# Kernel optimization log

Measured on AMD Instinct MI355X. Metric: run time of the kernel, lower is better.

The kernel has to match this reference:

```python
import jax, jax.numpy as jnp
import numpy as np

N = 100000
E = 1600000
F_IN, F_HID, F_OUT = 512, 512, 256
NEG_SLOPE = 0.01  # nn.LeakyReLU default


def setup_inputs() -> dict:
    key = jax.random.key(0)
    ks = jax.random.split(key, 16)
    def lin(k, fi, fo):
        s = 1.0 / np.sqrt(fi)
        return jax.random.uniform(k, (fi, fo), jnp.float32, -s, s)
    inp = {
        'x': jax.random.normal(ks[0], (N, F_IN), jnp.float32),
        'edge_index': jax.random.randint(ks[1], (2, E), 0, N, jnp.int64),
        'W1': lin(ks[2], F_IN, F_HID), 'b1': jnp.zeros((F_HID,), jnp.float32),
        'W2': lin(ks[3], F_HID, F_HID), 'b2': jnp.zeros((F_HID,), jnp.float32),
        'W3': lin(ks[4], F_HID, F_HID), 'b3': jnp.zeros((F_HID,), jnp.float32),
        'W4': lin(ks[5], F_HID, F_OUT), 'b4': jnp.zeros((F_OUT,), jnp.float32),
        'fcW1': lin(ks[6], F_OUT, 64), 'fcb1': jnp.zeros((64,), jnp.float32),
        'fcW2': lin(ks[7], 64, 1), 'fcb2': jnp.zeros((1,), jnp.float32),
    }
    return inp


def _gcn_norm(edge_index):
    # PyG gcn_norm with add_self_loops=True: deg counts incoming edges + 1 self loop
    src, dst = edge_index[0], edge_index[1]
    deg = jax.ops.segment_sum(jnp.ones((E,), jnp.float32), dst, num_segments=N) + 1.0
    dis = jax.lax.rsqrt(deg)  # deg >= 1 always (self loops)
    edge_norm = dis[src] * dis[dst]  # [E]
    self_norm = dis * dis            # [N], norm for the added self loop
    return src, dst, edge_norm, self_norm


def _gcn_layer(x, src, dst, edge_norm, self_norm, W, b):
    xw = x @ W  # transform-then-propagate (in < out not an issue here)
    agg = jax.ops.segment_sum(xw[src] * edge_norm[:, None], dst, num_segments=N)
    return agg + self_norm[:, None] * xw + b


def leaky(x):
    return jnp.where(x >= 0, x, NEG_SLOPE * x)


def reference(x, edge_index, W1, b1, W2, b2, W3, b3, W4, b4, fcW1, fcb1, fcW2, fcb2):
    src, dst, en, sn = _gcn_norm(edge_index)
    h = leaky(_gcn_layer(x, src, dst, en, sn, W1, b1))
    h = leaky(_gcn_layer(h, src, dst, en, sn, W2, b2))
    h = leaky(_gcn_layer(h, src, dst, en, sn, W3, b3))
    h = leaky(_gcn_layer(h, src, dst, en, sn, W4, b4))
    g = jnp.mean(h, axis=0, keepdims=True)  # global_mean_pool, batch=None -> [1, F_OUT]
    g = leaky(g @ fcW1 + fcb1)
    # dropout is identity in eval mode
    g = g @ fcW2 + fcb2
    return jax.nn.sigmoid(g)  # [1, 1]
```

## Files before the change

kernel.cpp:

```cpp
#include <hip/hip_runtime.h>
#include <hip/hip_bf16.h>
#include <cstdint>
#include <cstddef>


typedef unsigned short u16;
typedef unsigned char u8;
typedef unsigned int u32;
typedef u16 u16x4 __attribute__((ext_vector_type(4)));
typedef u16 u16x8 __attribute__((ext_vector_type(8)));
typedef u32 u32x2 __attribute__((ext_vector_type(2)));
typedef float f32x2 __attribute__((ext_vector_type(2)));
typedef float f32x4 __attribute__((ext_vector_type(4)));

__device__ __forceinline__ u16 f2bf(float f) {
  u32 u = __builtin_bit_cast(u32, f);
  u += 0x7fffu + ((u >> 16) & 1u);
  return (u16)(u >> 16);
}
__device__ __forceinline__ float bf2f(u16 h) {
  return __builtin_bit_cast(float, (u32)h << 16);
}
__device__ __forceinline__ void g2lds16(const void* g, void* l) {
  __builtin_amdgcn_global_load_lds((__attribute__((address_space(1))) void*)g,
                                   (__attribute__((address_space(3))) void*)l, 16, 0, 0);
}

__global__ __launch_bounds__(256) void init_kernel(int* __restrict__ deg,
                                                   int* __restrict__ cursor,
                                                   float* __restrict__ pool, int N) {
  int i = blockIdx.x * 256 + threadIdx.x;
  if (i < N) { deg[i] = 0; cursor[i] = 0; }
  if (i < 256) pool[i] = 0.f;
}

__global__ void detect_kernel(const int* __restrict__ ei, int* __restrict__ flag) {
  __shared__ int nz;
  if (threadIdx.x == 0) nz = 0;
  __syncthreads();
  if (ei[2 * threadIdx.x + 1] != 0) atomicAdd(&nz, 1);
  __syncthreads();
  if (threadIdx.x == 0) *flag = (nz == 0) ? 1 : 0;
}

__device__ __forceinline__ int ld_src(const int* ei, int E, int e, int f64) {
  return f64 ? (int)((const long long*)ei)[e] : ei[e];
}
__device__ __forceinline__ int ld_dst(const int* ei, int E, int e, int f64) {
  return f64 ? (int)((const long long*)ei)[(long long)E + e] : ei[E + e];
}

__global__ __launch_bounds__(256) void degree_kernel(const int* __restrict__ ei,
                                                     const int* __restrict__ flag,
                                                     int* __restrict__ deg, int E) {
  int e = blockIdx.x * 256 + threadIdx.x;
  if (e >= E) return;
  int f = *flag;
  atomicAdd(&deg[ld_dst(ei, E, e, f)], 1);
}

__global__ __launch_bounds__(256) void dis_kernel(const int* __restrict__ deg,
                                                  float* __restrict__ dis, int N) {
  int i = blockIdx.x * 256 + threadIdx.x;
  if (i < N) dis[i] = rsqrtf((float)deg[i] + 1.0f);
}

__global__ __launch_bounds__(1024) void scan1_kernel(const int* __restrict__ deg,
                                                     int* __restrict__ rs,
                                                     int* __restrict__ bsum, int N) {
  __shared__ int s[1024];
  int tid = threadIdx.x;
  int i = blockIdx.x * 1024 + tid;
  int v = (i < N) ? deg[i] : 0;
  s[tid] = v;
  __syncthreads();
  for (int off = 1; off < 1024; off <<= 1) {
    int t = (tid >= off) ? s[tid - off] : 0;
    __syncthreads();
    s[tid] += t;
    __syncthreads();
  }
  if (i < N) rs[i] = s[tid] - v;
  if (tid == 1023) bsum[blockIdx.x] = s[1023];
}

__global__ __launch_bounds__(1024) void scan2_kernel(const int* __restrict__ bsum,
                                                     int* __restrict__ boff, int nb) {
  __shared__ int s[1024];
  int tid = threadIdx.x;
  int v = (tid < nb) ? bsum[tid] : 0;
  s[tid] = v;
  __syncthreads();
  for (int off = 1; off < 1024; off <<= 1) {
    int t = (tid >= off) ? s[tid - off] : 0;
    __syncthreads();
    s[tid] += t;
    __syncthreads();
  }
  if (tid < nb) boff[tid] = s[tid] - v;
}

__global__ __launch_bounds__(256) void scan3_kernel(int* __restrict__ rs,
                                                    const int* __restrict__ boff, int N) {
  int i = blockIdx.x * 256 + threadIdx.x;
  if (i < N) rs[i] += boff[i >> 10];
}

__global__ __launch_bounds__(256) void fill_kernel(const int* __restrict__ ei,
                                                   const int* __restrict__ flag,
                                                   const int* __restrict__ rs,
                                                   int* __restrict__ cursor,
                                                   const float* __restrict__ dis,
                                                   u32x2* __restrict__ ev, int E) {
  int e = blockIdx.x * 256 + threadIdx.x;
  if (e >= E) return;
  int f = *flag;
  int s = ld_src(ei, E, e, f);
  int d = ld_dst(ei, E, e, f);
  int p = atomicAdd(&cursor[d], 1);
  float w = dis[s] * dis[d];
  u32x2 t;
  t.x = (u32)s;
  t.y = __builtin_bit_cast(u32, w);
  ev[rs[d] + p] = t;
}

__global__ __launch_bounds__(256) void convx_kernel(const float* __restrict__ x,
                                                    u8* __restrict__ x8, size_t n) {
  size_t i = ((size_t)blockIdx.x * 256 + threadIdx.x) * 4;
  if (i >= n) return;
  float4 v = *reinterpret_cast<const float4*>(x + i);
  int lo = __builtin_amdgcn_cvt_pk_fp8_f32(v.x, v.y, 0, false);
  int r = __builtin_amdgcn_cvt_pk_fp8_f32(v.z, v.w, lo, true);
  size_t row = i >> 9;
  int col = (int)(i & 511);
  int sw = ((int)(row & 7)) << 3;
  *reinterpret_cast<u32*>(x8 + row * 512 + (col ^ sw)) = (u32)r;
}

__global__ __launch_bounds__(256) void convw_kernel(const float* __restrict__ W,
                                                    u8* __restrict__ Wt, int Nout) {
  int id = blockIdx.x * 256 + threadIdx.x;
  if (id >= 512 * Nout) return;
  int k = id / Nout, nn = id - k * Nout;
  float v = W[id];
  int e = __builtin_amdgcn_cvt_pk_fp8_f32(v, v, 0, false);
  Wt[nn * 512 + (k ^ ((nn & 7) << 3))] = (u8)e;
}

__global__ __launch_bounds__(256, 4)
void gemm8_kernel(const u8* __restrict__ A, const u8* __restrict__ Bt,
                  u8* __restrict__ Cout, int M, int Nout, int gm, int lgy) {
  const int id = blockIdx.x;
  const int xcd = id & 7, q = id >> 3;
  const int by = q & ((1 << lgy) - 1);
  const int bx = ((q >> lgy) << 3) + xcd;
  if (bx >= gm) return;

  __shared__ u8 sA[128 * 64];
  __shared__ u8 sB[128 * 64];
  const int tid = threadIdx.x;
  const int wave = tid >> 6, lane = tid & 63;
  const int m0 = bx * 128;
  const int n0 = by * 128;
  const int wm = (wave >> 1) * 64, wn = (wave & 1) * 64;
  const int srow = tid >> 2;
  const int soff = (tid & 3) * 16;
  const int fr = lane & 15, fq8 = (lane >> 4) * 8;
  const int xa = (fr & 7) << 3;

  f32x4 acc[4][4];
#pragma unroll
  for (int i = 0; i < 4; ++i)
#pragma unroll
    for (int j = 0; j < 4; ++j) acc[i][j] = (f32x4){0.f, 0.f, 0.f, 0.f};

  int ar0 = m0 + srow;      if (ar0 >= M) ar0 = M - 1;
  int ar1 = m0 + 64 + srow; if (ar1 >= M) ar1 = M - 1;
  const size_t a0 = (size_t)ar0 * 512 + soff;
  const size_t a1 = (size_t)ar1 * 512 + soff;
  const size_t b0 = (size_t)(n0 + srow) * 512 + soff;
  const size_t b1 = (size_t)(n0 + 64 + srow) * 512 + soff;

  for (int k0 = 0; k0 < 512; k0 += 64) {
    g2lds16(A + a0 + k0, &sA[wave * 1024]);
    g2lds16(A + a1 + k0, &sA[4096 + wave * 1024]);
    g2lds16(Bt + b0 + k0, &sB[wave * 1024]);
    g2lds16(Bt + b1 + k0, &sB[4096 + wave * 1024]);
    __builtin_amdgcn_s_waitcnt(0);
    __syncthreads();

#pragma unroll
    for (int s = 0; s < 2; ++s) {
      long long af[4], bf[4];
#pragma unroll
      for (int t = 0; t < 4; ++t) {
        const int ra = (wm + t * 16 + fr) * 64;
        const int rb = (wn + t * 16 + fr) * 64;
        af[t] = *reinterpret_cast<const long long*>(&sA[ra + ((s * 32 + fq8) ^ xa)]);
        bf[t] = *reinterpret_cast<const long long*>(&sB[rb + ((s * 32 + fq8) ^ xa)]);
      }
#pragma unroll
      for (int i = 0; i < 4; ++i)
#pragma unroll
        for (int j = 0; j < 4; ++j)
          acc[i][j] = __builtin_amdgcn_mfma_f32_16x16x32_fp8_fp8(af[i], bf[j], acc[i][j], 0, 0, 0);
    }
    __syncthreads();
  }

  const int crow0 = m0 + wm + ((lane >> 4) << 2);
  const int ccol0 = n0 + wn + (lane & 15);
#pragma unroll
  for (int j = 0; j < 4; ++j) {
    const int col = ccol0 + j * 16;
#pragma unroll
    for (int i = 0; i < 4; ++i)
#pragma unroll
      for (int r = 0; r < 4; ++r) {
        int row = crow0 + i * 16 + r;
        if (row < M) {
          float v = acc[i][j][r];
          int e = __builtin_amdgcn_cvt_pk_fp8_f32(v, v, 0, false);
          Cout[(size_t)row * Nout + col] = (u8)e;
        }
      }
  }
}

__global__ __launch_bounds__(256)
void agg_kernel(const u8* __restrict__ xw, const u32x2* __restrict__ ev,
                const int* __restrict__ rs, const int* __restrict__ deg,
                const float* __restrict__ dis, const float* __restrict__ bias,
                u8* __restrict__ hout, int N) {
  const int wave = threadIdx.x >> 6;
  const int lane = threadIdx.x & 63;
  const int node = blockIdx.x * 4 + wave;
  if (node >= N) return;
  const int start = rs[node];
  const int d = deg[node];
  const float dd = dis[node];
  const int fo = lane * 8;

  f32x2 acc[4];
#pragma unroll
  for (int i = 0; i < 4; ++i) acc[i] = (f32x2){0.f, 0.f};

  const int total = d + 1;
  for (int base = 0; base < total; base += 64) {
    int t = base + lane;
    int s = node;
    float w = 0.f;
    if (t < d)       { u32x2 e = ev[start + t]; s = (int)e.x; w = __builtin_bit_cast(float, e.y); }
    else if (t == d) { w = dd * dd; }
    int cnt = total - base;
    if (cnt > 64) cnt = 64;
    int cnt8 = (cnt + 7) & ~7;
    int wi = __builtin_bit_cast(int, w);
    for (int j = 0; j < cnt8; j += 8) {
      u32x2 v[8];
      float ws[8];
#pragma unroll
      for (int k = 0; k < 8; ++k) {
        int sk = __builtin_amdgcn_readlane(s, j + k);
        ws[k] = __builtin_bit_cast(float, __builtin_amdgcn_readlane(wi, j + k));
        v[k] = *reinterpret_cast<const u32x2*>(xw + (size_t)sk * 512 + fo);
      }
#pragma unroll
      for (int k = 0; k < 8; ++k) {
        f32x2 p0 = __builtin_amdgcn_cvt_pk_f32_fp8((int)v[k].x, false);
        f32x2 p1 = __builtin_amdgcn_cvt_pk_f32_fp8((int)v[k].x, true);
        f32x2 p2 = __builtin_amdgcn_cvt_pk_f32_fp8((int)v[k].y, false);
        f32x2 p3 = __builtin_amdgcn_cvt_pk_f32_fp8((int)v[k].y, true);
        f32x2 wv = (f32x2){ws[k], ws[k]};
        acc[0] += wv * p0;
        acc[1] += wv * p1;
        acc[2] += wv * p2;
        acc[3] += wv * p3;
      }
    }
  }

  float h[8];
#pragma unroll
  for (int i = 0; i < 8; ++i) {
    float v = (i & 1) ? acc[i >> 1].y : acc[i >> 1].x;
    v += bias[fo + i];
    v = v >= 0.f ? v : 0.01f * v;
    h[i] = v;
  }
  int lo = __builtin_amdgcn_cvt_pk_fp8_f32(h[0], h[1], 0, false);
  lo = __builtin_amdgcn_cvt_pk_fp8_f32(h[2], h[3], lo, true);
  int hi = __builtin_amdgcn_cvt_pk_fp8_f32(h[4], h[5], 0, false);
  hi = __builtin_amdgcn_cvt_pk_fp8_f32(h[6], h[7], hi, true);
  u32x2 o; o.x = (u32)lo; o.y = (u32)hi;
  __builtin_nontemporal_store(o, reinterpret_cast<u32x2*>(
      hout + (size_t)node * 512 + (fo ^ ((node & 7) << 3))));
}

__global__ __launch_bounds__(256)
void agg256_kernel(const u8* __restrict__ xw, const u32x2* __restrict__ ev,
                   const int* __restrict__ rs, const int* __restrict__ deg,
                   const float* __restrict__ dis, const float* __restrict__ bias,
                   u16* __restrict__ hout, int N) {
  const int wave = threadIdx.x >> 6;
  const int lane = threadIdx.x & 63;
  const int node = blockIdx.x * 4 + wave;
  if (node >= N) return;
  const int start = rs[node];
  const int d = deg[node];
  const float dd = dis[node];
  const int fo = lane * 4;

  f32x2 acc[2];
  acc[0] = (f32x2){0.f, 0.f};
  acc[1] = (f32x2){0.f, 0.f};

  const int total = d + 1;
  for (int base = 0; base < total; base += 64) {
    int t = base + lane;
    int s = node;
    float w = 0.f;
    if (t < d)       { u32x2 e = ev[start + t]; s = (int)e.x; w = __builtin_bit_cast(float, e.y); }
    else if (t == d) { w = dd * dd; }
    int cnt = total - base;
    if (cnt > 64) cnt = 64;
    int cnt8 = (cnt + 7) & ~7;
    int wi = __builtin_bit_cast(int, w);
    for (int j = 0; j < cnt8; j += 8) {
      u32 v[8];
      float ws[8];
#pragma unroll
      for (int k = 0; k < 8; ++k) {
        int sk = __builtin_amdgcn_readlane(s, j + k);
        ws[k] = __builtin_bit_cast(float, __builtin_amdgcn_readlane(wi, j + k));
        v[k] = *reinterpret_cast<const u32*>(xw + (size_t)sk * 256 + fo);
      }
#pragma unroll
      for (int k = 0; k < 8; ++k) {
        f32x2 p0 = __builtin_amdgcn_cvt_pk_f32_fp8((int)v[k], false);
        f32x2 p1 = __builtin_amdgcn_cvt_pk_f32_fp8((int)v[k], true);
        f32x2 wv = (f32x2){ws[k], ws[k]};
        acc[0] += wv * p0;
        acc[1] += wv * p1;
      }
    }
  }

  u16x4 o;
#pragma unroll
  for (int i = 0; i < 4; ++i) {
    float v = (i & 1) ? acc[i >> 1].y : acc[i >> 1].x;
    v += bias[fo + i];
    v = v >= 0.f ? v : 0.01f * v;
    o[i] = f2bf(v);
  }
  *reinterpret_cast<u16x4*>(hout + (size_t)node * 256 + fo) = o;
}

__global__ __launch_bounds__(256) void pool_kernel(const u16* __restrict__ h,
                                                   float* __restrict__ pool, int N) {
  __shared__ float lds[8 * 256];
  const int tid = threadIdx.x;
  const int fg = tid & 31;
  const int rg = tid >> 5;
  float acc[8];
#pragma unroll
  for (int i = 0; i < 8; ++i) acc[i] = 0.f;
  for (int r = blockIdx.x * 8 + rg; r < N; r += gridDim.x * 8) {
    u16x8 v = *reinterpret_cast<const u16x8*>(h + (size_t)r * 256 + fg * 8);
#pragma unroll
    for (int i = 0; i < 8; ++i) acc[i] += bf2f(v[i]);
  }
#pragma unroll
  for (int i = 0; i < 8; ++i) lds[rg * 256 + fg * 8 + i] = acc[i];
  __syncthreads();
  float s = 0.f;
#pragma unroll
  for (int g = 0; g < 8; ++g) s += lds[g * 256 + tid];
  atomicAdd(&pool[tid], s);
}

__global__ void fc_kernel(const float* __restrict__ pool, const float* __restrict__ fcW1,
                          const float* __restrict__ fcb1, const float* __restrict__ fcW2,
                          const float* __restrict__ fcb2, float* __restrict__ out,
                          float invN) {
  int j = threadIdx.x;
  float acc = 0.f;
  for (int f = 0; f < 256; ++f) acc += pool[f] * invN * fcW1[f * 64 + j];
  float h = acc + fcb1[j];
  h = h >= 0.f ? h : 0.01f * h;
  float p = h * fcW2[j];
  for (int o = 32; o; o >>= 1) p += __shfl_down(p, o);
  if (j == 0) out[0] = 1.f / (1.f + expf(-(p + fcb2[0])));
}

extern "C" void kernel_launch(void* const* d_in, const int* in_sizes, int n_in,
                              void* d_out, int out_size, void* d_ws, size_t ws_size,
                              hipStream_t stream) {
  const float* x    = (const float*)d_in[0];
  const int*   ei   = (const int*)d_in[1];
  const float* W1   = (const float*)d_in[2];
  const float* b1   = (const float*)d_in[3];
  const float* W2   = (const float*)d_in[4];
  const float* b2   = (const float*)d_in[5];
  const float* W3   = (const float*)d_in[6];
  const float* b3   = (const float*)d_in[7];
  const float* W4   = (const float*)d_in[8];
  const float* b4   = (const float*)d_in[9];
  const float* fcW1 = (const float*)d_in[10];
  const float* fcb1 = (const float*)d_in[11];
  const float* fcW2 = (const float*)d_in[12];
  const float* fcb2 = (const float*)d_in[13];
  float* out = (float*)d_out;

  const int N = in_sizes[0] / 512;
  const int E = in_sizes[1] / 2;

  char* p = (char*)d_ws;
  auto carve = [&](size_t bytes) {
    char* r = p;
    p += (bytes + 255) & ~(size_t)255;
    return r;
  };
  u8*  bufX = (u8*)carve((size_t)N * 512);
  u8*  bufP = (u8*)carve((size_t)N * 512);
  u8*  bufQ = (u8*)carve((size_t)N * 512);
  u16* bufH4 = (u16*)carve((size_t)N * 256 * 2);
  u8* Wt1 = (u8*)carve(512 * 512);
  u8* Wt2 = (u8*)carve(512 * 512);
  u8* Wt3 = (u8*)carve(512 * 512);
  u8* Wt4 = (u8*)carve(512 * 256);
  int* deg    = (int*)carve((size_t)N * 4);
  int* cursor = (int*)carve((size_t)N * 4);
  int* rs     = (int*)carve((size_t)(N + 1) * 4);
  u32x2* ev   = (u32x2*)carve((size_t)E * 8);
  int* bsum   = (int*)carve(1024 * 4);
  int* boff   = (int*)carve(1024 * 4);
  int* flag   = (int*)carve(256);
  float* disv = (float*)carve((size_t)N * 4);
  float* pool = (float*)carve(256 * 4);
  if ((size_t)(p - (char*)d_ws) > ws_size) return;

  const int nb1024 = (N + 1023) / 1024;

  init_kernel<<<(N + 255) / 256, 256, 0, stream>>>(deg, cursor, pool, N);
  detect_kernel<<<1, 256, 0, stream>>>(ei, flag);
  degree_kernel<<<(E + 255) / 256, 256, 0, stream>>>(ei, flag, deg, E);
  dis_kernel<<<(N + 255) / 256, 256, 0, stream>>>(deg, disv, N);
  scan1_kernel<<<nb1024, 1024, 0, stream>>>(deg, rs, bsum, N);
  scan2_kernel<<<1, 1024, 0, stream>>>(bsum, boff, nb1024);
  scan3_kernel<<<(N + 255) / 256, 256, 0, stream>>>(rs, boff, N);
  fill_kernel<<<(E + 255) / 256, 256, 0, stream>>>(ei, flag, rs, cursor, disv, ev, E);

  convx_kernel<<<((size_t)N * 512 / 4 + 255) / 256, 256, 0, stream>>>(x, bufX, (size_t)N * 512);
  convw_kernel<<<(512 * 512 + 255) / 256, 256, 0, stream>>>(W1, Wt1, 512);
  convw_kernel<<<(512 * 512 + 255) / 256, 256, 0, stream>>>(W2, Wt2, 512);
  convw_kernel<<<(512 * 512 + 255) / 256, 256, 0, stream>>>(W3, Wt3, 512);
  convw_kernel<<<(512 * 256 + 255) / 256, 256, 0, stream>>>(W4, Wt4, 256);

  const int gm = (N + 127) / 128;
  const int gm8 = (gm + 7) & ~7;
  const unsigned ga = (unsigned)((N + 3) / 4);

  gemm8_kernel<<<gm8 * 4, 256, 0, stream>>>(bufX, Wt1, bufP, N, 512, gm, 2);
  agg_kernel<<<ga, 256, 0, stream>>>(bufP, ev, rs, deg, disv, b1, bufQ, N);
  gemm8_kernel<<<gm8 * 4, 256, 0, stream>>>(bufQ, Wt2, bufP, N, 512, gm, 2);
  agg_kernel<<<ga, 256, 0, stream>>>(bufP, ev, rs, deg, disv, b2, bufX, N);
  gemm8_kernel<<<gm8 * 4, 256, 0, stream>>>(bufX, Wt3, bufP, N, 512, gm, 2);
  agg_kernel<<<ga, 256, 0, stream>>>(bufP, ev, rs, deg, disv, b3, bufQ, N);
  gemm8_kernel<<<gm8 * 2, 256, 0, stream>>>(bufQ, Wt4, bufP, N, 256, gm, 1);
  agg256_kernel<<<ga, 256, 0, stream>>>(bufP, ev, rs, deg, disv, b4, bufH4, N);

  pool_kernel<<<256, 256, 0, stream>>>(bufH4, pool, N);
  fc_kernel<<<1, 64, 0, stream>>>(pool, fcW1, fcb1, fcW2, fcb2, out, 1.0f / (float)N);
}
```

Measured before the change: 1.107 ms.

## Double-buffer LDS tiles in fp8 GEMM to overlap global loads with MFMA

```diff
diff --git a/kernel.cpp b/kernel.cpp
--- a/kernel.cpp
+++ b/kernel.cpp
@@ -148,7 +148,7 @@
   Wt[nn * 512 + (k ^ ((nn & 7) << 3))] = (u8)e;
 }
 
-__global__ __launch_bounds__(256, 4)
+__global__ __launch_bounds__(256, 3)
 void gemm8_kernel(const u8* __restrict__ A, const u8* __restrict__ Bt,
                   u8* __restrict__ Cout, int M, int Nout, int gm, int lgy) {
   const int id = blockIdx.x;
@@ -157,14 +157,12 @@
   const int bx = ((q >> lgy) << 3) + xcd;
   if (bx >= gm) return;
 
-  __shared__ u8 sA[128 * 64];
-  __shared__ u8 sB[128 * 64];
+  __shared__ u8 smem[32768];
   const int tid = threadIdx.x;
   const int wave = tid >> 6, lane = tid & 63;
   const int m0 = bx * 128;
   const int n0 = by * 128;
   const int wm = (wave >> 1) * 64, wn = (wave & 1) * 64;
-  const int srow = tid >> 2;
   const int soff = (tid & 3) * 16;
   const int fr = lane & 15, fq8 = (lane >> 4) * 8;
   const int xa = (fr & 7) << 3;
@@ -175,30 +173,46 @@
 #pragma unroll
     for (int j = 0; j < 4; ++j) acc[i][j] = (f32x4){0.f, 0.f, 0.f, 0.f};
 
+  const int srow = tid >> 2;
   int ar0 = m0 + srow;      if (ar0 >= M) ar0 = M - 1;
   int ar1 = m0 + 64 + srow; if (ar1 >= M) ar1 = M - 1;
   const size_t a0 = (size_t)ar0 * 512 + soff;
   const size_t a1 = (size_t)ar1 * 512 + soff;
   const size_t b0 = (size_t)(n0 + srow) * 512 + soff;
   const size_t b1 = (size_t)(n0 + 64 + srow) * 512 + soff;
-
-  for (int k0 = 0; k0 < 512; k0 += 64) {
-    g2lds16(A + a0 + k0, &sA[wave * 1024]);
-    g2lds16(A + a1 + k0, &sA[4096 + wave * 1024]);
-    g2lds16(Bt + b0 + k0, &sB[wave * 1024]);
-    g2lds16(Bt + b1 + k0, &sB[4096 + wave * 1024]);
-    __builtin_amdgcn_s_waitcnt(0);
-    __syncthreads();
-
+  const int wofs = wave * 1024;
+
+  {
+    g2lds16(A + a0, &smem[wofs]);
+    g2lds16(A + a1, &smem[4096 + wofs]);
+    g2lds16(Bt + b0, &smem[16384 + wofs]);
+    g2lds16(Bt + b1, &smem[16384 + 4096 + wofs]);
+  }
+  __builtin_amdgcn_s_waitcnt(0);
+  __syncthreads();
+
+  int cur = 0;
+  for (int t = 0; t < 8; ++t) {
+    if (t < 7) {
+      const int k1 = (t + 1) * 64;
+      const int nb = (cur ^ 1) * 8192;
+      g2lds16(A + a0 + k1, &smem[nb + wofs]);
+      g2lds16(A + a1 + k1, &smem[nb + 4096 + wofs]);
+      g2lds16(Bt + b0 + k1, &smem[16384 + nb + wofs]);
+      g2lds16(Bt + b1 + k1, &smem[16384 + nb + 4096 + wofs]);
+    }
+
+    const u8* sA = &smem[cur * 8192];
+    const u8* sB = &smem[16384 + cur * 8192];
 #pragma unroll
     for (int s = 0; s < 2; ++s) {
       long long af[4], bf[4];
 #pragma unroll
-      for (int t = 0; t < 4; ++t) {
-        const int ra = (wm + t * 16 + fr) * 64;
-        const int rb = (wn + t * 16 + fr) * 64;
-        af[t] = *reinterpret_cast<const long long*>(&sA[ra + ((s * 32 + fq8) ^ xa)]);
-        bf[t] = *reinterpret_cast<const long long*>(&sB[rb + ((s * 32 + fq8) ^ xa)]);
+      for (int t4 = 0; t4 < 4; ++t4) {
+        const int ra = (wm + t4 * 16 + fr) * 64;
+        const int rb = (wn + t4 * 16 + fr) * 64;
+        af[t4] = *reinterpret_cast<const long long*>(&sA[ra + ((s * 32 + fq8) ^ xa)]);
+        bf[t4] = *reinterpret_cast<const long long*>(&sB[rb + ((s * 32 + fq8) ^ xa)]);
       }
 #pragma unroll
       for (int i = 0; i < 4; ++i)
@@ -206,7 +220,10 @@
         for (int j = 0; j < 4; ++j)
           acc[i][j] = __builtin_amdgcn_mfma_f32_16x16x32_fp8_fp8(af[i], bf[j], acc[i][j], 0, 0, 0);
     }
+
+    __builtin_amdgcn_s_waitcnt(0);
     __syncthreads();
+    cur ^= 1;
   }
 
   const int crow0 = m0 + wm + ((lane >> 4) << 2);
```

Measured after the change: 1.094 ms. About the same (-1.2%).
